# Performance work log

Hardware: AMD Instinct MI355X
Metric: run time of the kernel (lower is better)

The kernel has to match this reference:

```python
import jax, jax.numpy as jnp
import numpy as np
from jax import lax

M_RANGE = 1  # padding = m_range, kernel is (2*m_range+1)^2 = 9 classes of 3x3


def _conv(x, kernel):
    # torch F.conv2d (cross-correlation), stride 1, padding M_RANGE
    return lax.conv_general_dilated(
        x, kernel, window_strides=(1, 1),
        padding=[(M_RANGE, M_RANGE), (M_RANGE, M_RANGE)],
        dimension_numbers=('NCHW', 'OIHW', 'NCHW'))


def _construct_seg(ones, m_mask, m_kernel):
    # ones.expand_as(m_mask) * m_mask, then per-sample conv2d -> batched conv
    return _conv(ones * m_mask, m_kernel)  # [B,1,H,W]


def _construct_image(im, m_mask, appear, m_kernel):
    # im: [B,C,H,W]; m_mask: [B,K,H,W]; appear: [B,1,H,W]
    im = im * appear
    B, C, H, W = im.shape
    K = m_mask.shape[1]
    # fuse the python double loop: fold (B,C) into batch, conv K->1 once
    im_expand = (im[:, :, None, :, :] * m_mask[:, None, :, :, :]).reshape(B * C, K, H, W)
    return _conv(im_expand, m_kernel).reshape(B, C, H, W)


def setup_inputs() -> dict:
    key = jax.random.key(0)
    k0, k1, k2, k3 = jax.random.split(key, 4)
    B, C, H, W, K, N_INPUTS = 32, 3, 256, 256, 9, 2
    im_input_f = jax.random.uniform(k0, (B, N_INPUTS * C, H, W), dtype=jnp.float32)
    im_input_b = jax.random.uniform(k1, (B, N_INPUTS * C, H, W), dtype=jnp.float32)
    ones = jnp.ones((B, 1, H, W), dtype=jnp.float32)
    # gt motion masks: soft per-pixel distribution over K motion classes
    gt_motion_f = jax.nn.softmax(jax.random.normal(k2, (B, K, H, W), dtype=jnp.float32), axis=1)
    gt_motion_b = jax.nn.softmax(jax.random.normal(k3, (B, K, H, W), dtype=jnp.float32), axis=1)
    # one-hot displacement kernels: kernel i has a 1 at flat position i of the 3x3 window
    m_kernel = jnp.eye(K, dtype=jnp.float32).reshape(K, 3, 3)[None]  # [1,K,3,3]
    return {"im_input_f": im_input_f, "im_input_b": im_input_b, "ones": ones,
            "gt_motion_f": gt_motion_f, "gt_motion_b": gt_motion_b, "m_kernel": m_kernel}


def reference(im_input_f, im_input_b, ones, gt_motion_f, gt_motion_b, m_kernel):
    IM_CHANNEL = 3
    relu = jax.nn.relu
    m_mask_f, m_mask_b = gt_motion_f, gt_motion_b

    seg_f = _construct_seg(ones, m_mask_f, m_kernel)
    seg_b = _construct_seg(ones, m_mask_b, m_kernel)

    disappear_f = relu(seg_f - 1)
    appear_f = relu(1 - disappear_f)
    disappear_b = relu(seg_b - 1)
    appear_b = relu(1 - disappear_b)

    pred_f = _construct_image(im_input_f[:, -IM_CHANNEL:, :, :], m_mask_f, appear_f, m_kernel)
    pred_b = _construct_image(im_input_b[:, -IM_CHANNEL:, :, :], m_mask_b, appear_b, m_kernel)

    seg_f = 1 - relu(1 - seg_f)
    seg_b = 1 - relu(1 - seg_b)
    attn = (seg_f + 1e-5) / (seg_f + seg_b + 2e-5)  # [B,1,H,W], broadcasts over C
    pred = attn * pred_f + (1 - attn) * pred_b
    return (pred, m_mask_f, 1 - appear_f, attn, m_mask_b, 1 - appear_b, 1 - attn)
```

## Files before the change

kernel.cpp:

```cpp
#include <hip/hip_runtime.h>

#define BB 32
#define KK 9
#define CC 3
#define HH 256
#define WW 256
#define HW (HH * WW)
#define NPIX (BB * HW)

#define SZ_P ((size_t)BB * CC * HW)
#define SZ_M ((size_t)BB * KK * HW)
#define SZ_S ((size_t)BB * HW)

__global__ __launch_bounds__(256) void seg_attn_kernel(
    const float* __restrict__ gt_f, const float* __restrict__ gt_b,
    float* __restrict__ out) {
  int idx = blockIdx.x * blockDim.x + threadIdx.x;
  if (idx >= NPIX) return;
  int b  = idx >> 16;
  int hw = idx & (HW - 1);
  int h  = hw >> 8;
  int w  = hw & (WW - 1);

  const float* gf = gt_f + (size_t)b * KK * HW;
  const float* gb = gt_b + (size_t)b * KK * HW;

  float seg_f = 0.f, seg_b = 0.f;
#pragma unroll
  for (int k = 0; k < KK; ++k) {
    int y = h + (k / 3) - 1;
    int x = w + (k % 3) - 1;
    if (y >= 0 && y < HH && x >= 0 && x < WW) {
      int off = k * HW + (y << 8) + x;
      seg_f += gf[off];
      seg_b += gb[off];
    }
  }

  float dis_f = fmaxf(seg_f - 1.f, 0.f);
  float app_f = fmaxf(1.f - dis_f, 0.f);
  float dis_b = fmaxf(seg_b - 1.f, 0.f);
  float app_b = fmaxf(1.f - dis_b, 0.f);
  float sfc = 1.f - fmaxf(1.f - seg_f, 0.f);
  float sbc = 1.f - fmaxf(1.f - seg_b, 0.f);
  float attn = (sfc + 1e-5f) / (sfc + sbc + 2e-5f);

  float* o_disf   = out + SZ_P + SZ_M;
  float* o_attn   = out + SZ_P + SZ_M + SZ_S;
  float* o_disb   = out + SZ_P + 2 * SZ_M + 2 * SZ_S;
  float* o_1mattn = out + SZ_P + 2 * SZ_M + 3 * SZ_S;

  o_disf[idx]   = 1.f - app_f;
  o_attn[idx]   = attn;
  o_disb[idx]   = 1.f - app_b;
  o_1mattn[idx] = 1.f - attn;
}

__global__ __launch_bounds__(256) void pred_kernel(
    const float* __restrict__ im_f, const float* __restrict__ im_b,
    const float* __restrict__ gt_f, const float* __restrict__ gt_b,
    float* __restrict__ out) {
  int idx = blockIdx.x * blockDim.x + threadIdx.x;
  if (idx >= NPIX) return;
  int b  = idx >> 16;
  int hw = idx & (HW - 1);
  int h  = hw >> 8;
  int w  = hw & (WW - 1);

  const float* o_disf = out + SZ_P + SZ_M;
  const float* o_attn = out + SZ_P + SZ_M + SZ_S;
  const float* o_disb = out + SZ_P + 2 * SZ_M + 2 * SZ_S;

  const float* gf  = gt_f + (size_t)b * KK * HW;
  const float* gb  = gt_b + (size_t)b * KK * HW;
  const float* imf = im_f + ((size_t)b * 6 + 3) * HW;
  const float* imb = im_b + ((size_t)b * 6 + 3) * HW;
  const float* dfb = o_disf + (size_t)b * HW;
  const float* dbb = o_disb + (size_t)b * HW;

  float attn = o_attn[idx];

  float pf0 = 0.f, pf1 = 0.f, pf2 = 0.f;
  float pb0 = 0.f, pb1 = 0.f, pb2 = 0.f;
#pragma unroll
  for (int k = 0; k < KK; ++k) {
    int y = h + (k / 3) - 1;
    int x = w + (k % 3) - 1;
    if (y >= 0 && y < HH && x >= 0 && x < WW) {
      int p = (y << 8) + x;
      float af = 1.f - dfb[p];
      float cf = af * gf[k * HW + p];
      pf0 = fmaf(cf, imf[p], pf0);
      pf1 = fmaf(cf, imf[HW + p], pf1);
      pf2 = fmaf(cf, imf[2 * HW + p], pf2);
      float ab = 1.f - dbb[p];
      float cb = ab * gb[k * HW + p];
      pb0 = fmaf(cb, imb[p], pb0);
      pb1 = fmaf(cb, imb[HW + p], pb1);
      pb2 = fmaf(cb, imb[2 * HW + p], pb2);
    }
  }

  float at2 = 1.f - attn;
  size_t base = (size_t)b * CC * HW + hw;
  out[base]          = attn * pf0 + at2 * pb0;
  out[base + HW]     = attn * pf1 + at2 * pb1;
  out[base + 2 * HW] = attn * pf2 + at2 * pb2;
}

extern "C" void kernel_launch(void* const* d_in, const int* in_sizes, int n_in,
                              void* d_out, int out_size, void* d_ws, size_t ws_size,
                              hipStream_t stream) {
  const float* im_f = (const float*)d_in[0];
  const float* im_b = (const float*)d_in[1];
  const float* gt_f = (const float*)d_in[3];
  const float* gt_b = (const float*)d_in[4];
  float* out = (float*)d_out;

  dim3 block(256);
  dim3 grid(NPIX / 256);

  hipMemcpyAsync(out + SZ_P, gt_f, SZ_M * sizeof(float),
                 hipMemcpyDeviceToDevice, stream);
  hipMemcpyAsync(out + SZ_P + SZ_M + 2 * SZ_S, gt_b, SZ_M * sizeof(float),
                 hipMemcpyDeviceToDevice, stream);

  seg_attn_kernel<<<grid, block, 0, stream>>>(gt_f, gt_b, out);
  pred_kernel<<<grid, block, 0, stream>>>(im_f, im_b, gt_f, gt_b, out);
}
```

Measured before the change: 443.2 us.

## Fuse seg/attn, prediction and mask copies into one tiled kernel

Merges the two per-pixel kernels and both device-to-device mask copies into a single kernel over 64x16 spatial tiles. Seg sums for each tile plus a one-pixel halo are computed into shared memory and reused for the appearance weights of neighbours, instead of being written to global memory and re-read. The mask copies are done inside the kernel from the gt values it already loads. This removes extra launches, the copy passes and the global round trip of intermediates, at the cost of recomputing halo seg values and adding a block barrier.

```diff
diff --git a/kernel.cpp b/kernel.cpp
--- a/kernel.cpp
+++ b/kernel.cpp
@@ -6,106 +6,125 @@
 #define HH 256
 #define WW 256
 #define HW (HH * WW)
-#define NPIX (BB * HW)
 
 #define SZ_P ((size_t)BB * CC * HW)
 #define SZ_M ((size_t)BB * KK * HW)
 #define SZ_S ((size_t)BB * HW)
 
-__global__ __launch_bounds__(256) void seg_attn_kernel(
-    const float* __restrict__ gt_f, const float* __restrict__ gt_b,
-    float* __restrict__ out) {
-  int idx = blockIdx.x * blockDim.x + threadIdx.x;
-  if (idx >= NPIX) return;
-  int b  = idx >> 16;
-  int hw = idx & (HW - 1);
-  int h  = hw >> 8;
-  int w  = hw & (WW - 1);
+#define TX 64
+#define TY 16
+#define TILES_X (WW / TX)
+#define TILES_Y (HH / TY)
+#define TILES_PER_B (TILES_X * TILES_Y)
 
-  const float* gf = gt_f + (size_t)b * KK * HW;
-  const float* gb = gt_b + (size_t)b * KK * HW;
-
-  float seg_f = 0.f, seg_b = 0.f;
-#pragma unroll
-  for (int k = 0; k < KK; ++k) {
-    int y = h + (k / 3) - 1;
-    int x = w + (k % 3) - 1;
-    if (y >= 0 && y < HH && x >= 0 && x < WW) {
-      int off = k * HW + (y << 8) + x;
-      seg_f += gf[off];
-      seg_b += gb[off];
-    }
-  }
-
-  float dis_f = fmaxf(seg_f - 1.f, 0.f);
-  float app_f = fmaxf(1.f - dis_f, 0.f);
-  float dis_b = fmaxf(seg_b - 1.f, 0.f);
-  float app_b = fmaxf(1.f - dis_b, 0.f);
-  float sfc = 1.f - fmaxf(1.f - seg_f, 0.f);
-  float sbc = 1.f - fmaxf(1.f - seg_b, 0.f);
-  float attn = (sfc + 1e-5f) / (sfc + sbc + 2e-5f);
-
-  float* o_disf   = out + SZ_P + SZ_M;
-  float* o_attn   = out + SZ_P + SZ_M + SZ_S;
-  float* o_disb   = out + SZ_P + 2 * SZ_M + 2 * SZ_S;
-  float* o_1mattn = out + SZ_P + 2 * SZ_M + 3 * SZ_S;
-
-  o_disf[idx]   = 1.f - app_f;
-  o_attn[idx]   = attn;
-  o_disb[idx]   = 1.f - app_b;
-  o_1mattn[idx] = 1.f - attn;
-}
-
-__global__ __launch_bounds__(256) void pred_kernel(
+__global__ __launch_bounds__(256) void fused_binet_kernel(
     const float* __restrict__ im_f, const float* __restrict__ im_b,
     const float* __restrict__ gt_f, const float* __restrict__ gt_b,
     float* __restrict__ out) {
-  int idx = blockIdx.x * blockDim.x + threadIdx.x;
-  if (idx >= NPIX) return;
-  int b  = idx >> 16;
-  int hw = idx & (HW - 1);
-  int h  = hw >> 8;
-  int w  = hw & (WW - 1);
+  __shared__ float s_sf[TY + 2][TX + 2];
+  __shared__ float s_sb[TY + 2][TX + 2];
 
-  const float* o_disf = out + SZ_P + SZ_M;
-  const float* o_attn = out + SZ_P + SZ_M + SZ_S;
-  const float* o_disb = out + SZ_P + 2 * SZ_M + 2 * SZ_S;
+  int bid = blockIdx.x;
+  int b = bid / TILES_PER_B;
+  int t = bid % TILES_PER_B;
+  int ty0 = (t / TILES_X) * TY;
+  int tx0 = (t % TILES_X) * TX;
 
   const float* gf  = gt_f + (size_t)b * KK * HW;
   const float* gb  = gt_b + (size_t)b * KK * HW;
   const float* imf = im_f + ((size_t)b * 6 + 3) * HW;
   const float* imb = im_b + ((size_t)b * 6 + 3) * HW;
-  const float* dfb = o_disf + (size_t)b * HW;
-  const float* dbb = o_disb + (size_t)b * HW;
 
-  float attn = o_attn[idx];
+  int tid = threadIdx.x;
 
-  float pf0 = 0.f, pf1 = 0.f, pf2 = 0.f;
-  float pb0 = 0.f, pb1 = 0.f, pb2 = 0.f;
+  for (int i = tid; i < (TY + 2) * (TX + 2); i += 256) {
+    int ly = i / (TX + 2);
+    int lx = i - ly * (TX + 2);
+    int y = ty0 + ly - 1;
+    int x = tx0 + lx - 1;
+    float sf = 0.f, sb = 0.f;
+    if (y >= 0 && y < HH && x >= 0 && x < WW) {
 #pragma unroll
-  for (int k = 0; k < KK; ++k) {
-    int y = h + (k / 3) - 1;
-    int x = w + (k % 3) - 1;
-    if (y >= 0 && y < HH && x >= 0 && x < WW) {
-      int p = (y << 8) + x;
-      float af = 1.f - dfb[p];
-      float cf = af * gf[k * HW + p];
-      pf0 = fmaf(cf, imf[p], pf0);
-      pf1 = fmaf(cf, imf[HW + p], pf1);
-      pf2 = fmaf(cf, imf[2 * HW + p], pf2);
-      float ab = 1.f - dbb[p];
-      float cb = ab * gb[k * HW + p];
-      pb0 = fmaf(cb, imb[p], pb0);
-      pb1 = fmaf(cb, imb[HW + p], pb1);
-      pb2 = fmaf(cb, imb[2 * HW + p], pb2);
+      for (int k = 0; k < KK; ++k) {
+        int yy = y + (k / 3) - 1;
+        int xx = x + (k % 3) - 1;
+        if (yy >= 0 && yy < HH && xx >= 0 && xx < WW) {
+          int off = k * HW + (yy << 8) + xx;
+          sf += gf[off];
+          sb += gb[off];
+        }
+      }
     }
+    s_sf[ly][lx] = sf;
+    s_sb[ly][lx] = sb;
   }
+  __syncthreads();
 
-  float at2 = 1.f - attn;
-  size_t base = (size_t)b * CC * HW + hw;
-  out[base]          = attn * pf0 + at2 * pb0;
-  out[base + HW]     = attn * pf1 + at2 * pb1;
-  out[base + 2 * HW] = attn * pf2 + at2 * pb2;
+  float* o_mf     = out + SZ_P;
+  float* o_disf   = out + SZ_P + SZ_M;
+  float* o_attn   = o_disf + SZ_S;
+  float* o_mb     = o_attn + SZ_S;
+  float* o_disb   = o_mb + SZ_M;
+  float* o_1mattn = o_disb + SZ_S;
+
+  int lx  = tid & (TX - 1);
+  int ly0 = tid >> 6;
+
+#pragma unroll
+  for (int r = 0; r < 4; ++r) {
+    int ly = ly0 + r * 4;
+    int h = ty0 + ly;
+    int w = tx0 + lx;
+    int hw = (h << 8) + w;
+    size_t sidx = (size_t)b * HW + hw;
+
+    float sf = s_sf[ly + 1][lx + 1];
+    float sb = s_sb[ly + 1][lx + 1];
+    float dis_f = fmaxf(sf - 1.f, 0.f);
+    float app_f = fmaxf(1.f - dis_f, 0.f);
+    float dis_b = fmaxf(sb - 1.f, 0.f);
+    float app_b = fmaxf(1.f - dis_b, 0.f);
+    float sfc = 1.f - fmaxf(1.f - sf, 0.f);
+    float sbc = 1.f - fmaxf(1.f - sb, 0.f);
+    float attn = (sfc + 1e-5f) / (sfc + sbc + 2e-5f);
+
+    o_disf[sidx]   = 1.f - app_f;
+    o_attn[sidx]   = attn;
+    o_disb[sidx]   = 1.f - app_b;
+    o_1mattn[sidx] = 1.f - attn;
+
+    float pf0 = 0.f, pf1 = 0.f, pf2 = 0.f;
+    float pb0 = 0.f, pb1 = 0.f, pb2 = 0.f;
+#pragma unroll
+    for (int k = 0; k < KK; ++k) {
+      size_t moff = (size_t)b * KK * HW + (size_t)k * HW + hw;
+      o_mf[moff] = gf[k * HW + hw];
+      o_mb[moff] = gb[k * HW + hw];
+
+      int y = h + (k / 3) - 1;
+      int x = w + (k % 3) - 1;
+      if (y >= 0 && y < HH && x >= 0 && x < WW) {
+        int p = (y << 8) + x;
+        float sfq = s_sf[ly + (k / 3)][lx + (k % 3)];
+        float af = fmaxf(1.f - fmaxf(sfq - 1.f, 0.f), 0.f);
+        float cf = af * gf[k * HW + p];
+        pf0 = fmaf(cf, imf[p], pf0);
+        pf1 = fmaf(cf, imf[HW + p], pf1);
+        pf2 = fmaf(cf, imf[2 * HW + p], pf2);
+        float sbq = s_sb[ly + (k / 3)][lx + (k % 3)];
+        float ab = fmaxf(1.f - fmaxf(sbq - 1.f, 0.f), 0.f);
+        float cb = ab * gb[k * HW + p];
+        pb0 = fmaf(cb, imb[p], pb0);
+        pb1 = fmaf(cb, imb[HW + p], pb1);
+        pb2 = fmaf(cb, imb[2 * HW + p], pb2);
+      }
+    }
+    float at2 = 1.f - attn;
+    size_t pbase = (size_t)b * CC * HW + hw;
+    out[pbase]          = fmaf(attn, pf0, at2 * pb0);
+    out[pbase + HW]     = fmaf(attn, pf1, at2 * pb1);
+    out[pbase + 2 * HW] = fmaf(attn, pf2, at2 * pb2);
+  }
 }
 
 extern "C" void kernel_launch(void* const* d_in, const int* in_sizes, int n_in,
@@ -118,13 +137,7 @@
   float* out = (float*)d_out;
 
   dim3 block(256);
-  dim3 grid(NPIX / 256);
+  dim3 grid(BB * TILES_PER_B);
 
-  hipMemcpyAsync(out + SZ_P, gt_f, SZ_M * sizeof(float),
-                 hipMemcpyDeviceToDevice, stream);
-  hipMemcpyAsync(out + SZ_P + SZ_M + 2 * SZ_S, gt_b, SZ_M * sizeof(float),
-                 hipMemcpyDeviceToDevice, stream);
-
-  seg_attn_kernel<<<grid, block, 0, stream>>>(gt_f, gt_b, out);
-  pred_kernel<<<grid, block, 0, stream>>>(im_f, im_b, gt_f, gt_b, out);
+  fused_binet_kernel<<<grid, block, 0, stream>>>(im_f, im_b, gt_f, gt_b, out);
 }
```

After: 458.0 us. 3.3% more time.

## Fuse mask copies into seg kernel and vectorize both kernels with float4 and shuffles

Applied to the files above, without the earlier changes.

Removes the two device-to-device memcpys of the motion masks and writes those outputs from the seg kernel, which already reads the masks, so each mask is read once. Both kernels now process four horizontally adjacent pixels per thread with float4 loads, and the horizontal neighbours come from wavefront shuffles instead of extra unaligned loads. Non-temporal stores are used for write-once outputs, and blocks are swizzled. The cost is more register pressure and more complex boundary handling. The seg kernel still reloads the masks for the off-centre rows.

```diff
diff --git a/kernel.cpp b/kernel.cpp
--- a/kernel.cpp
+++ b/kernel.cpp
@@ -6,106 +6,192 @@
 #define HH 256
 #define WW 256
 #define HW (HH * WW)
-#define NPIX (BB * HW)
 
 #define SZ_P ((size_t)BB * CC * HW)
 #define SZ_M ((size_t)BB * KK * HW)
 #define SZ_S ((size_t)BB * HW)
 
-__global__ __launch_bounds__(256) void seg_attn_kernel(
+typedef float f4 __attribute__((ext_vector_type(4)));
+
+__device__ __forceinline__ f4 ld4(const float* p) { return *(const f4*)p; }
+__device__ __forceinline__ void st4(float* p, f4 v) { *(f4*)p = v; }
+__device__ __forceinline__ void ntst4(float* p, f4 v) {
+  __builtin_nontemporal_store(v, (f4*)p);
+}
+__device__ __forceinline__ f4 vmax(f4 a, f4 b) {
+  return __builtin_elementwise_max(a, b);
+}
+__device__ __forceinline__ f4 win(f4 v, float l, float r, int dx) {
+  if (dx == 0) return (f4){l, v.x, v.y, v.z};
+  if (dx == 2) return (f4){v.y, v.z, v.w, r};
+  return v;
+}
+
+__device__ __forceinline__ void decode(int bid, int tid, int& b, int& y,
+                                       int& lane, int& x0) {
+  int actual = ((bid & 7) << 8) | (bid >> 3);
+  b = actual >> 6;
+  int q = actual & 63;
+  lane = tid & 63;
+  y = (q << 2) + (tid >> 6);
+  x0 = lane << 2;
+}
+
+__global__ __launch_bounds__(256) void seg_mask_kernel(
     const float* __restrict__ gt_f, const float* __restrict__ gt_b,
     float* __restrict__ out) {
-  int idx = blockIdx.x * blockDim.x + threadIdx.x;
-  if (idx >= NPIX) return;
-  int b  = idx >> 16;
-  int hw = idx & (HW - 1);
-  int h  = hw >> 8;
-  int w  = hw & (WW - 1);
+  int b, y, lane, x0;
+  decode(blockIdx.x, threadIdx.x, b, y, lane, x0);
+  size_t hw = ((size_t)y << 8) + x0;
 
   const float* gf = gt_f + (size_t)b * KK * HW;
   const float* gb = gt_b + (size_t)b * KK * HW;
 
-  float seg_f = 0.f, seg_b = 0.f;
+  float* o_mf     = out + SZ_P;
+  float* o_disf   = out + SZ_P + SZ_M;
+  float* o_attn   = o_disf + SZ_S;
+  float* o_mb     = o_attn + SZ_S;
+  float* o_disb   = o_mb + SZ_M;
+  float* o_1mattn = o_disb + SZ_S;
+
+  f4 segf = {0.f, 0.f, 0.f, 0.f};
+  f4 segb = {0.f, 0.f, 0.f, 0.f};
+
 #pragma unroll
   for (int k = 0; k < KK; ++k) {
-    int y = h + (k / 3) - 1;
-    int x = w + (k % 3) - 1;
-    if (y >= 0 && y < HH && x >= 0 && x < WW) {
-      int off = k * HW + (y << 8) + x;
-      seg_f += gf[off];
-      seg_b += gb[off];
-    }
+    const int dy = k / 3, dx = k % 3;
+    int yr = y + dy - 1;
+    bool rowok = (unsigned)yr < HH;
+    f4 vf = {0.f, 0.f, 0.f, 0.f}, vb = {0.f, 0.f, 0.f, 0.f};
+    if (rowok) {
+      size_t off = (size_t)k * HW + ((size_t)yr << 8) + x0;
+      vf = ld4(gf + off);
+      vb = ld4(gb + off);
+    }
+    f4 wf, wb;
+    if (dx == 1) {
+      wf = vf; wb = vb;
+    } else if (dx == 0) {
+      float lf = __shfl_up(vf.w, 1), lb = __shfl_up(vb.w, 1);
+      if (lane == 0) { lf = 0.f; lb = 0.f; }
+      wf = (f4){lf, vf.x, vf.y, vf.z};
+      wb = (f4){lb, vb.x, vb.y, vb.z};
+    } else {
+      float rf = __shfl_down(vf.x, 1), rb = __shfl_down(vb.x, 1);
+      if (lane == 63) { rf = 0.f; rb = 0.f; }
+      wf = (f4){vf.y, vf.z, vf.w, rf};
+      wb = (f4){vb.y, vb.z, vb.w, rb};
+    }
+    segf += wf;
+    segb += wb;
+
+    f4 cf = vf, cb = vb;
+    if (dy != 1) {
+      cf = ld4(gf + (size_t)k * HW + hw);
+      cb = ld4(gb + (size_t)k * HW + hw);
+    }
+    size_t moff = (size_t)b * KK * HW + (size_t)k * HW + hw;
+    ntst4(o_mf + moff, cf);
+    ntst4(o_mb + moff, cb);
   }
 
-  float dis_f = fmaxf(seg_f - 1.f, 0.f);
-  float app_f = fmaxf(1.f - dis_f, 0.f);
-  float dis_b = fmaxf(seg_b - 1.f, 0.f);
-  float app_b = fmaxf(1.f - dis_b, 0.f);
-  float sfc = 1.f - fmaxf(1.f - seg_f, 0.f);
-  float sbc = 1.f - fmaxf(1.f - seg_b, 0.f);
-  float attn = (sfc + 1e-5f) / (sfc + sbc + 2e-5f);
-
-  float* o_disf   = out + SZ_P + SZ_M;
-  float* o_attn   = out + SZ_P + SZ_M + SZ_S;
-  float* o_disb   = out + SZ_P + 2 * SZ_M + 2 * SZ_S;
-  float* o_1mattn = out + SZ_P + 2 * SZ_M + 3 * SZ_S;
-
-  o_disf[idx]   = 1.f - app_f;
-  o_attn[idx]   = attn;
-  o_disb[idx]   = 1.f - app_b;
-  o_1mattn[idx] = 1.f - attn;
+  f4 one = {1.f, 1.f, 1.f, 1.f}, zero = {0.f, 0.f, 0.f, 0.f};
+  f4 disf = vmax(segf - one, zero);
+  f4 appf = vmax(one - disf, zero);
+  f4 disb = vmax(segb - one, zero);
+  f4 appb = vmax(one - disb, zero);
+  f4 sfc = one - vmax(one - segf, zero);
+  f4 sbc = one - vmax(one - segb, zero);
+  f4 attn = (sfc + 1e-5f) / (sfc + sbc + 2e-5f);
+
+  size_t sidx = (size_t)b * HW + hw;
+  st4(o_disf + sidx, one - appf);
+  st4(o_attn + sidx, attn);
+  st4(o_disb + sidx, one - appb);
+  ntst4(o_1mattn + sidx, one - attn);
 }
 
 __global__ __launch_bounds__(256) void pred_kernel(
     const float* __restrict__ im_f, const float* __restrict__ im_b,
     const float* __restrict__ gt_f, const float* __restrict__ gt_b,
     float* __restrict__ out) {
-  int idx = blockIdx.x * blockDim.x + threadIdx.x;
-  if (idx >= NPIX) return;
-  int b  = idx >> 16;
-  int hw = idx & (HW - 1);
-  int h  = hw >> 8;
-  int w  = hw & (WW - 1);
-
-  const float* o_disf = out + SZ_P + SZ_M;
-  const float* o_attn = out + SZ_P + SZ_M + SZ_S;
-  const float* o_disb = out + SZ_P + 2 * SZ_M + 2 * SZ_S;
+  int b, y, lane, x0;
+  decode(blockIdx.x, threadIdx.x, b, y, lane, x0);
+  size_t hw = ((size_t)y << 8) + x0;
 
   const float* gf  = gt_f + (size_t)b * KK * HW;
   const float* gb  = gt_b + (size_t)b * KK * HW;
   const float* imf = im_f + ((size_t)b * 6 + 3) * HW;
   const float* imb = im_b + ((size_t)b * 6 + 3) * HW;
-  const float* dfb = o_disf + (size_t)b * HW;
-  const float* dbb = o_disb + (size_t)b * HW;
-
-  float attn = o_attn[idx];
-
-  float pf0 = 0.f, pf1 = 0.f, pf2 = 0.f;
-  float pb0 = 0.f, pb1 = 0.f, pb2 = 0.f;
+  const float* dfp = out + SZ_P + SZ_M + (size_t)b * HW;
+  const float* atp = out + SZ_P + SZ_M + SZ_S + (size_t)b * HW;
+  const float* dbp = out + SZ_P + 2 * SZ_M + 2 * SZ_S + (size_t)b * HW;
+
+  f4 z = {0.f, 0.f, 0.f, 0.f};
+  f4 pf0 = z, pf1 = z, pf2 = z, pb0 = z, pb1 = z, pb2 = z;
+
 #pragma unroll
-  for (int k = 0; k < KK; ++k) {
-    int y = h + (k / 3) - 1;
-    int x = w + (k % 3) - 1;
-    if (y >= 0 && y < HH && x >= 0 && x < WW) {
-      int p = (y << 8) + x;
-      float af = 1.f - dfb[p];
-      float cf = af * gf[k * HW + p];
-      pf0 = fmaf(cf, imf[p], pf0);
-      pf1 = fmaf(cf, imf[HW + p], pf1);
-      pf2 = fmaf(cf, imf[2 * HW + p], pf2);
-      float ab = 1.f - dbb[p];
-      float cb = ab * gb[k * HW + p];
-      pb0 = fmaf(cb, imb[p], pb0);
-      pb1 = fmaf(cb, imb[HW + p], pb1);
-      pb2 = fmaf(cb, imb[2 * HW + p], pb2);
+  for (int dy = 0; dy < 3; ++dy) {
+    int yr = y + dy - 1;
+    bool rowok = (unsigned)yr < HH;
+    size_t rbase = ((size_t)yr << 8) + x0;
+
+    f4 dfv = z, dbv = z;
+    f4 if0 = z, if1 = z, if2 = z, ib0 = z, ib1 = z, ib2 = z;
+    if (rowok) {
+      dfv = ld4(dfp + rbase);
+      dbv = ld4(dbp + rbase);
+      if0 = ld4(imf + rbase);
+      if1 = ld4(imf + HW + rbase);
+      if2 = ld4(imf + 2 * HW + rbase);
+      ib0 = ld4(imb + rbase);
+      ib1 = ld4(imb + HW + rbase);
+      ib2 = ld4(imb + 2 * HW + rbase);
+    }
+    f4 aff = 1.f - dfv;
+    f4 afb = 1.f - dbv;
+    float affl = __shfl_up(aff.w, 1),  affr = __shfl_down(aff.x, 1);
+    float afbl = __shfl_up(afb.w, 1),  afbr = __shfl_down(afb.x, 1);
+    float if0l = __shfl_up(if0.w, 1),  if0r = __shfl_down(if0.x, 1);
+    float if1l = __shfl_up(if1.w, 1),  if1r = __shfl_down(if1.x, 1);
+    float if2l = __shfl_up(if2.w, 1),  if2r = __shfl_down(if2.x, 1);
+    float ib0l = __shfl_up(ib0.w, 1),  ib0r = __shfl_down(ib0.x, 1);
+    float ib1l = __shfl_up(ib1.w, 1),  ib1r = __shfl_down(ib1.x, 1);
+    float ib2l = __shfl_up(ib2.w, 1),  ib2r = __shfl_down(ib2.x, 1);
+
+#pragma unroll
+    for (int dx = 0; dx < 3; ++dx) {
+      const int k = 3 * dy + dx;
+      f4 gfv = z, gbv = z;
+      if (rowok) {
+        gfv = ld4(gf + (size_t)k * HW + rbase);
+        gbv = ld4(gb + (size_t)k * HW + rbase);
+      }
+      float gfl = 0.f, gfr = 0.f, gbl = 0.f, gbr = 0.f;
+      if (dx == 0) {
+        gfl = __shfl_up(gfv.w, 1); gbl = __shfl_up(gbv.w, 1);
+        if (lane == 0) { gfl = 0.f; gbl = 0.f; }
+      } else if (dx == 2) {
+        gfr = __shfl_down(gfv.x, 1); gbr = __shfl_down(gbv.x, 1);
+        if (lane == 63) { gfr = 0.f; gbr = 0.f; }
+      }
+      f4 cf = win(aff, affl, affr, dx) * win(gfv, gfl, gfr, dx);
+      f4 cb = win(afb, afbl, afbr, dx) * win(gbv, gbl, gbr, dx);
+      pf0 += cf * win(if0, if0l, if0r, dx);
+      pf1 += cf * win(if1, if1l, if1r, dx);
+      pf2 += cf * win(if2, if2l, if2r, dx);
+      pb0 += cb * win(ib0, ib0l, ib0r, dx);
+      pb1 += cb * win(ib1, ib1l, ib1r, dx);
+      pb2 += cb * win(ib2, ib2l, ib2r, dx);
     }
   }
 
-  float at2 = 1.f - attn;
-  size_t base = (size_t)b * CC * HW + hw;
-  out[base]          = attn * pf0 + at2 * pb0;
-  out[base + HW]     = attn * pf1 + at2 * pb1;
-  out[base + 2 * HW] = attn * pf2 + at2 * pb2;
+  f4 attn = ld4(atp + hw);
+  f4 at2 = 1.f - attn;
+  size_t pbase = (size_t)b * CC * HW + hw;
+  ntst4(out + pbase,          attn * pf0 + at2 * pb0);
+  ntst4(out + pbase + HW,     attn * pf1 + at2 * pb1);
+  ntst4(out + pbase + 2 * HW, attn * pf2 + at2 * pb2);
 }
 
 extern "C" void kernel_launch(void* const* d_in, const int* in_sizes, int n_in,
@@ -118,13 +204,8 @@
   float* out = (float*)d_out;
 
   dim3 block(256);
-  dim3 grid(NPIX / 256);
-
-  hipMemcpyAsync(out + SZ_P, gt_f, SZ_M * sizeof(float),
-                 hipMemcpyDeviceToDevice, stream);
-  hipMemcpyAsync(out + SZ_P + SZ_M + 2 * SZ_S, gt_b, SZ_M * sizeof(float),
-                 hipMemcpyDeviceToDevice, stream);
-
-  seg_attn_kernel<<<grid, block, 0, stream>>>(gt_f, gt_b, out);
+  dim3 grid(BB * 64);
+
+  seg_mask_kernel<<<grid, block, 0, stream>>>(gt_f, gt_b, out);
   pred_kernel<<<grid, block, 0, stream>>>(im_f, im_b, gt_f, gt_b, out);
 }
```

New measurement: 403.9 us. 1.1x faster.
